# Kernel tuning notes

Hardware: AMD Instinct MI355X
Metric: run time of the kernel (lower is better)

## Reference

```python
import jax, jax.numpy as jnp
import numpy as np

N, E, F, H, C, G, NC = 50000, 800000, 128, 3, 64, 16, 10
NEG_SLOPE = 0.2


def gatv2_layer(x, src, dst, Wl, Wr, att, b, concat):
    # PyG GATv2Conv (share_weights=False, add_self_loops already in src/dst)
    n = x.shape[0]
    h, c = att.shape
    xl = (x @ Wl).reshape(n, h, c)   # source-side transform
    xr = (x @ Wr).reshape(n, h, c)   # target-side transform
    # per-edge attention logits: a^T LeakyReLU(xl_j + xr_i)
    e = jax.nn.leaky_relu(xl[src] + xr[dst], NEG_SLOPE)          # [E,h,c]
    logits = jnp.einsum('ehc,hc->eh', e, att)                    # [E,h]
    # segment softmax over incoming edges of each target node
    m = jax.ops.segment_max(logits, dst, num_segments=n)
    m = jnp.where(jnp.isfinite(m), m, jnp.zeros_like(m))
    p = jnp.exp(logits - m[dst])
    denom = jax.ops.segment_sum(p, dst, num_segments=n)
    alpha = p / jnp.maximum(denom[dst], 1e-16)                   # [E,h]
    out = jax.ops.segment_sum(alpha[:, :, None] * xl[src], dst, num_segments=n)
    out = out.reshape(n, h * c) if concat else out.mean(axis=1)
    return out + b


def setup_inputs() -> dict:
    key = jax.random.key(0)
    ks = jax.random.split(key, 16)
    glorot = lambda k, shp: jax.random.normal(k, shp, jnp.float32) * np.sqrt(2.0 / (shp[0] + shp[-1]))
    return {
        'x': jax.random.normal(ks[0], (N, F), jnp.float32),
        'edge_index': jax.random.randint(ks[1], (2, E), 0, N, jnp.int64),
        'batch': jnp.sort(jax.random.randint(ks[2], (N,), 0, G, jnp.int64)),
        'Wl1': glorot(ks[3], (F, H * C)),
        'Wr1': glorot(ks[4], (F, H * C)),
        'att1': glorot(ks[5], (H, C)),
        'b1': jnp.zeros((H * C,), jnp.float32),
        'Wl2': glorot(ks[6], (H * C, H * C)),
        'Wr2': glorot(ks[7], (H * C, H * C)),
        'att2': glorot(ks[8], (H, C)),
        'b2': jnp.zeros((C,), jnp.float32),
        'Wc': glorot(ks[9], (C, NC)),
        'bc': jnp.zeros((NC,), jnp.float32),
    }


def reference(x, edge_index, batch, Wl1, Wr1, att1, b1, Wl2, Wr2, att2, b2, Wc, bc):
    n = x.shape[0]
    loops = jnp.arange(n, dtype=edge_index.dtype)
    src = jnp.concatenate([edge_index[0], loops])  # add self loops (PyG default)
    dst = jnp.concatenate([edge_index[1], loops])
    h = jax.nn.relu(gatv2_layer(x, src, dst, Wl1, Wr1, att1, b1, True))
    # dropout is identity in eval mode
    h = jax.nn.relu(gatv2_layer(h, src, dst, Wl2, Wr2, att2, b2, False))
    # global mean pool over graph ids
    sums = jax.ops.segment_sum(h, batch, num_segments=G)
    counts = jax.ops.segment_sum(jnp.ones((n, 1), h.dtype), batch, num_segments=G)
    pooled = sums / jnp.maximum(counts, 1.0)
    logits = pooled @ Wc + bc
    return jax.nn.softmax(logits, axis=1)
```

## Files before the change

### kernel.cpp

```cpp
#include <hip/hip_runtime.h>
#include <hip/hip_bf16.h>
#include <stdint.h>

#define NN 50000
#define EE 800000
#define FF 128
#define HH 3
#define CC 64
#define GG 16
#define NCLS 10
#define HC (HH*CC)

#define LOG2E 1.4426950408889634f

typedef uint16_t u16;
typedef __attribute__((ext_vector_type(8))) short short8;
typedef __attribute__((ext_vector_type(4))) float f32x4;

__device__ __forceinline__ u16 bf16_rne(float x) {
    uint32_t u = __float_as_uint(x);
    u += 0x7fffu + ((u >> 16) & 1u);
    return (u16)(u >> 16);
}
__device__ __forceinline__ void split2(float x, u16& h, u16& l) {
    h = bf16_rne(x);
    float fh = __uint_as_float((uint32_t)h << 16);
    l = bf16_rne(x - fh);
}

__device__ __forceinline__ float qsum16(float x) {
    #define DPP_ADD(ctrl) \
        x += __int_as_float(__builtin_amdgcn_update_dpp(0, __float_as_int(x), ctrl, 0xf, 0xf, true))
    DPP_ADD(0x111);
    DPP_ADD(0x112);
    DPP_ADD(0x114);
    DPP_ADD(0x118);
    #undef DPP_ADD
    return __int_as_float(__builtin_amdgcn_ds_swizzle(__float_as_int(x), 0x1F0));
}

__device__ __forceinline__ void unpack12(uint4 q0, uint4 q1, float v[3][4]) {
    v[0][0] = __uint_as_float(q0.x << 16);
    v[1][0] = __uint_as_float(q0.x & 0xffff0000u);
    v[2][0] = __uint_as_float(q0.y << 16);
    v[0][1] = __uint_as_float(q0.z << 16);
    v[1][1] = __uint_as_float(q0.z & 0xffff0000u);
    v[2][1] = __uint_as_float(q0.w << 16);
    v[0][2] = __uint_as_float(q1.x << 16);
    v[1][2] = __uint_as_float(q1.x & 0xffff0000u);
    v[2][2] = __uint_as_float(q1.y << 16);
    v[0][3] = __uint_as_float(q1.z << 16);
    v[1][3] = __uint_as_float(q1.z & 0xffff0000u);
    v[2][3] = __uint_as_float(q1.w << 16);
}

__global__ void count_deg(const int* __restrict__ dst, int* __restrict__ deg, int E) {
    int i = blockIdx.x * blockDim.x + threadIdx.x;
    if (i < E) atomicAdd(&deg[dst[i]], 1);
}

__global__ __launch_bounds__(256) void scan_local(const int* __restrict__ deg,
                                                  int* __restrict__ rowp1,
                                                  int* __restrict__ partials, int n) {
    __shared__ int sums[256];
    int base = blockIdx.x * 2048 + threadIdx.x * 8;
    int v[8]; int run = 0;
    #pragma unroll
    for (int i = 0; i < 8; ++i) {
        int x = (base + i < n) ? deg[base + i] : 0;
        run += x; v[i] = run;
    }
    sums[threadIdx.x] = run;
    __syncthreads();
    for (int off = 1; off < 256; off <<= 1) {
        int t = (threadIdx.x >= off) ? sums[threadIdx.x - off] : 0;
        __syncthreads();
        sums[threadIdx.x] += t;
        __syncthreads();
    }
    int prefix = (threadIdx.x > 0) ? sums[threadIdx.x - 1] : 0;
    #pragma unroll
    for (int i = 0; i < 8; ++i)
        if (base + i < n) rowp1[base + i] = v[i] + prefix;
    if (threadIdx.x == 255) partials[blockIdx.x] = sums[255];
}

__global__ void scan_partials(int* partials, int nb) {
    if (threadIdx.x == 0 && blockIdx.x == 0) {
        int run = 0;
        for (int b = 0; b < nb; ++b) { int t = partials[b]; partials[b] = run; run += t; }
    }
}

__global__ void scan_finish(int* __restrict__ rowp, int* __restrict__ cursor,
                            const int* __restrict__ partials, int n) {
    int i = blockIdx.x * blockDim.x + threadIdx.x;
    if (i == 0) { rowp[0] = 0; cursor[0] = 0; }
    if (i < n) {
        int v = rowp[1 + i] + partials[i / 2048];
        rowp[1 + i] = v;
        if (i < n - 1) cursor[i + 1] = v;
    }
}

__global__ void fill_csr(const int* __restrict__ src, const int* __restrict__ dst,
                         int* __restrict__ cursor, int* __restrict__ colv, int E) {
    int i = blockIdx.x * blockDim.x + threadIdx.x;
    if (i < E) {
        int pos = atomicAdd(&cursor[dst[i]], 1);
        colv[pos] = src[i];
    }
}

__global__ void prep_all(const float* __restrict__ Wl1, const float* __restrict__ Wr1,
                         const float* __restrict__ Wl2, const float* __restrict__ Wr2,
                         u16* l1h, u16* l1l, u16* r1h, u16* r1l,
                         u16* l2h, u16* l2l, u16* r2h, u16* r2l) {
    int idx = blockIdx.x * blockDim.x + threadIdx.x;
    const int S1 = FF * HC, S2 = HC * HC;
    const float* B; u16 *H, *L; int K, f;
    if (idx < S1)                { B = Wl1; H = l1h; L = l1l; K = FF; f = idx; }
    else if (idx < 2*S1)         { B = Wr1; H = r1h; L = r1l; K = FF; f = idx - S1; }
    else if (idx < 2*S1 + S2)    { B = Wl2; H = l2h; L = l2l; K = HC; f = idx - 2*S1; }
    else if (idx < 2*S1 + 2*S2)  { B = Wr2; H = r2h; L = r2l; K = HC; f = idx - 2*S1 - S2; }
    else return;
    const int KB = K / 32;
    int j    = f & 7;
    int lane = (f >> 3) & 63;
    int rest = f >> 9;
    int kb    = rest % KB;
    int ntile = rest / KB;
    int n = ntile * 16 + (lane & 15);
    int k = kb * 32 + (lane >> 4) * 8 + j;
    u16 h, l; split2(B[k * HC + n], h, l);
    H[f] = h;
    L[f] = l;
}

template<int K, bool SPLITIN>
__global__ __launch_bounds__(256) void mfma_gemm(
    const float* __restrict__ Af,
    const u16* __restrict__ Ahi, const u16* __restrict__ Alo,
    const u16* __restrict__ B1h, const u16* __restrict__ B1l,
    const u16* __restrict__ B2h, const u16* __restrict__ B2l,
    u16* __restrict__ C1p, u16* __restrict__ C2p, int M)
{
    constexpr int KB  = K / 32;
    constexpr int NCH = K / 8;
    __shared__ __align__(16) u16 smem[64 * K * 2];
    u16* Ah = smem;
    u16* Al = smem + 64 * K;

    const int tid  = threadIdx.x;
    const int w    = tid >> 6;
    const int lane = tid & 63;
    const int m0   = blockIdx.x * 64;

    #pragma unroll
    for (int i = 0; i < (64 * NCH) / 256; ++i) {
        int id   = tid + 256 * i;
        int row  = id & 63;
        int c    = id >> 6;
        int rt   = row >> 4, frow = row & 15;
        int kb   = c >> 2,   fkc  = c & 3;
        int sw   = (rt ^ (rt << 1)) & 7;
        int slot = (fkc * 16 + frow) ^ sw;
        int laddr = ((rt * KB + kb) * 64 + slot) * 8;
        int grow = min(m0 + row, M - 1);
        if constexpr (SPLITIN) {
            float4 a0 = *(const float4*)(Af + (size_t)grow * K + c * 8);
            float4 a1 = *(const float4*)(Af + (size_t)grow * K + c * 8 + 4);
            ushort4 h0, l0, h1, l1;
            split2(a0.x, h0.x, l0.x); split2(a0.y, h0.y, l0.y);
            split2(a0.z, h0.z, l0.z); split2(a0.w, h0.w, l0.w);
            split2(a1.x, h1.x, l1.x); split2(a1.y, h1.y, l1.y);
            split2(a1.z, h1.z, l1.z); split2(a1.w, h1.w, l1.w);
            *(ushort4*)&Ah[laddr]     = h0;
            *(ushort4*)&Ah[laddr + 4] = h1;
            *(ushort4*)&Al[laddr]     = l0;
            *(ushort4*)&Al[laddr + 4] = l1;
        } else {
            *(uint4*)&Ah[laddr] = *(const uint4*)(Ahi + (size_t)grow * K + c * 8);
            *(uint4*)&Al[laddr] = *(const uint4*)(Alo + (size_t)grow * K + c * 8);
        }
    }
    __syncthreads();

    f32x4 acc[2][3][4];
    #pragma unroll
    for (int mt = 0; mt < 2; ++mt)
        #pragma unroll
        for (int nt = 0; nt < 3; ++nt)
            #pragma unroll
            for (int rt = 0; rt < 4; ++rt)
                acc[mt][nt][rt] = (f32x4){0.f, 0.f, 0.f, 0.f};

    const u16* bbase[2][3][2];
    #pragma unroll
    for (int mt = 0; mt < 2; ++mt) {
        const u16* Bh = mt ? B2h : B1h;
        const u16* Bl = mt ? B2l : B1l;
        #pragma unroll
        for (int nt = 0; nt < 3; ++nt) {
            size_t o = ((size_t)(w * 3 + nt) * KB * 64 + lane) * 8;
            bbase[mt][nt][0] = Bh + o;
            bbase[mt][nt][1] = Bl + o;
        }
    }

    #pragma unroll 2
    for (int kb = 0; kb < KB; ++kb) {
        short8 afh[4], afl[4];
        #pragma unroll
        for (int rt = 0; rt < 4; ++rt) {
            int sw = (rt ^ (rt << 1)) & 7;
            int laddr = ((rt * KB + kb) * 64 + (lane ^ sw)) * 8;
            afh[rt] = *(const short8*)&Ah[laddr];
            afl[rt] = *(const short8*)&Al[laddr];
        }
        #pragma unroll
        for (int mt = 0; mt < 2; ++mt) {
            #pragma unroll
            for (int nt = 0; nt < 3; ++nt) {
                short8 bh = *(const short8*)(bbase[mt][nt][0] + kb * 512);
                short8 bl = *(const short8*)(bbase[mt][nt][1] + kb * 512);
                #pragma unroll
                for (int rt = 0; rt < 4; ++rt)
                    acc[mt][nt][rt] = __builtin_amdgcn_mfma_f32_16x16x32_bf16(afh[rt], bh, acc[mt][nt][rt], 0, 0, 0);
                #pragma unroll
                for (int rt = 0; rt < 4; ++rt)
                    acc[mt][nt][rt] = __builtin_amdgcn_mfma_f32_16x16x32_bf16(afh[rt], bl, acc[mt][nt][rt], 0, 0, 0);
                #pragma unroll
                for (int rt = 0; rt < 4; ++rt)
                    acc[mt][nt][rt] = __builtin_amdgcn_mfma_f32_16x16x32_bf16(afl[rt], bh, acc[mt][nt][rt], 0, 0, 0);
            }
        }
    }

    const int frow = lane & 15;
    const int q4   = (lane >> 4) * 4;
    #pragma unroll
    for (int mt = 0; mt < 2; ++mt) {
        __syncthreads();
        #pragma unroll
        for (int nt = 0; nt < 3; ++nt) {
            int col = w * 48 + nt * 16 + frow;
            int c = col & 63, h = col >> 6;
            int u = c * 4 + h;
            int chunk = u >> 3, within = u & 7;
            #pragma unroll
            for (int rt = 0; rt < 4; ++rt)
                #pragma unroll
                for (int r = 0; r < 4; ++r) {
                    int lrow = rt * 16 + q4 + r;
                    smem[lrow * 256 + ((chunk ^ (lrow & 7)) << 3) + within] =
                        bf16_rne(acc[mt][nt][rt][r]);
                }
        }
        __syncthreads();
        u16* C = mt ? C2p : C1p;
        #pragma unroll
        for (int i = 0; i < 8; ++i) {
            int idx  = tid + 256 * i;
            int lrow = idx >> 5;
            int coff = idx & 31;
            if (m0 + lrow < M)
                *(uint4*)(C + (size_t)(m0 + lrow) * 256 + coff * 8) =
                    *(const uint4*)&smem[lrow * 256 + ((coff ^ (lrow & 7)) << 3)];
        }
    }
}

template<bool MASK>
__device__ __forceinline__ void gat_quad(
    int i0, int q, int l, int beg, int cnt, int cm1, int cmax, int node,
    const int* __restrict__ colv, const u16* __restrict__ xlp,
    const float attv[3][4], const float xrv[3][4],
    float s[3], float acc[3][4])
{
    int idx = i0 + q;
    int iq  = min(idx, cmax);
    int cs  = colv[beg + iq];
    int src = (idx < cm1) ? cs : node;
    const u16* p = xlp + ((size_t)src << 8) + (l << 4);
    uint4 q0 = *(const uint4*)p;
    uint4 q1 = *(const uint4*)(p + 8);
    float v[3][4];
    unpack12(q0, q1, v);
    #pragma unroll
    for (int r = 0; r < 3; ++r) {
        float t0 = v[r][0] + xrv[r][0]; t0 = fmaxf(t0, 0.2f * t0);
        float t1 = v[r][1] + xrv[r][1]; t1 = fmaxf(t1, 0.2f * t1);
        float t2 = v[r][2] + xrv[r][2]; t2 = fmaxf(t2, 0.2f * t2);
        float t3 = v[r][3] + xrv[r][3]; t3 = fmaxf(t3, 0.2f * t3);
        float d = t0 * attv[r][0];
        d = fmaf(t1, attv[r][1], d);
        d = fmaf(t2, attv[r][2], d);
        d = fmaf(t3, attv[r][3], d);
        d = qsum16(d);
        float pe = __builtin_amdgcn_exp2f(d);
        if (MASK) pe = (idx < cnt) ? pe : 0.f;
        s[r] += pe;
        acc[r][0] = fmaf(pe, v[r][0], acc[r][0]);
        acc[r][1] = fmaf(pe, v[r][1], acc[r][1]);
        acc[r][2] = fmaf(pe, v[r][2], acc[r][2]);
        acc[r][3] = fmaf(pe, v[r][3], acc[r][3]);
    }
}

template<int CONCAT>
__global__ __launch_bounds__(256) void gat_agg(
    const u16* __restrict__ xlp, const u16* __restrict__ xrp,
    const int* __restrict__ rowp, const int* __restrict__ colv,
    const float* __restrict__ att, const float* __restrict__ bias,
    float* __restrict__ out, u16* __restrict__ ohi, u16* __restrict__ olo, int n)
{
    const int wave = threadIdx.x >> 6;
    const int lane = threadIdx.x & 63;
    const int node = __builtin_amdgcn_readfirstlane(blockIdx.x * 4 + wave);
    if (node >= n) return;
    const int q = lane >> 4;
    const int l = lane & 15;

    float attv[3][4], xrv[3][4];
    #pragma unroll
    for (int r = 0; r < 3; ++r) {
        float4 a4 = *(const float4*)(att + r * 64 + 4 * l);
        attv[r][0] = a4.x * LOG2E; attv[r][1] = a4.y * LOG2E;
        attv[r][2] = a4.z * LOG2E; attv[r][3] = a4.w * LOG2E;
    }
    {
        uint4 x0 = *(const uint4*)(xrp + ((size_t)node << 8) + (l << 4));
        uint4 x1 = *(const uint4*)(xrp + ((size_t)node << 8) + (l << 4) + 8);
        unpack12(x0, x1, xrv);
    }

    float s[3] = {0.f, 0.f, 0.f};
    float acc[3][4] = {{0.f}};

    const int beg  = rowp[node];
    const int cnt  = rowp[node + 1] - beg + 1;
    const int cm1  = cnt - 1;
    const int cmax = max(cnt - 2, 0);

    int i0 = 0;
    const int nfull = cnt & ~3;
    for (; i0 < nfull; i0 += 4)
        gat_quad<false>(i0, q, l, beg, cnt, cm1, cmax, node, colv, xlp, attv, xrv, s, acc);
    if (i0 < cnt)
        gat_quad<true>(i0, q, l, beg, cnt, cm1, cmax, node, colv, xlp, attv, xrv, s, acc);

    #pragma unroll
    for (int r = 0; r < 3; ++r) {
        s[r] += __shfl_xor(s[r], 16, 64);
        s[r] += __shfl_xor(s[r], 32, 64);
        #pragma unroll
        for (int j = 0; j < 4; ++j) {
            acc[r][j] += __shfl_xor(acc[r][j], 16, 64);
            acc[r][j] += __shfl_xor(acc[r][j], 32, 64);
        }
    }

    if (CONCAT) {
        if (lane < 48) {
            int r = lane >> 4, ll = lane & 15;
            float inv = 1.f / s[r];
            float4 bv = *(const float4*)(bias + r * 64 + 4 * ll);
            ushort4 hv, lv;
            float o0 = fmaxf(fmaf(acc[r][0], inv, bv.x), 0.f); split2(o0, hv.x, lv.x);
            float o1 = fmaxf(fmaf(acc[r][1], inv, bv.y), 0.f); split2(o1, hv.y, lv.y);
            float o2 = fmaxf(fmaf(acc[r][2], inv, bv.z), 0.f); split2(o2, hv.z, lv.z);
            float o3 = fmaxf(fmaf(acc[r][3], inv, bv.w), 0.f); split2(o3, hv.w, lv.w);
            size_t ob = (size_t)node * HC + r * 64 + 4 * ll;
            *(ushort4*)&ohi[ob] = hv;
            *(ushort4*)&olo[ob] = lv;
        }
    } else {
        if (lane < 16) {
            float i0v = 1.f / s[0], i1v = 1.f / s[1], i2v = 1.f / s[2];
            float4 bv = *(const float4*)(bias + 4 * l);
            float4 o;
            o.x = fmaxf((acc[0][0]*i0v + acc[1][0]*i1v + acc[2][0]*i2v) * (1.f/3.f) + bv.x, 0.f);
            o.y = fmaxf((acc[0][1]*i0v + acc[1][1]*i1v + acc[2][1]*i2v) * (1.f/3.f) + bv.y, 0.f);
            o.z = fmaxf((acc[0][2]*i0v + acc[1][2]*i1v + acc[2][2]*i2v) * (1.f/3.f) + bv.z, 0.f);
            o.w = fmaxf((acc[0][3]*i0v + acc[1][3]*i1v + acc[2][3]*i2v) * (1.f/3.f) + bv.w, 0.f);
            *(float4*)&out[(size_t)node * CC + 4 * l] = o;
        }
    }
}

#define POOL_BLOCKS 384
__global__ __launch_bounds__(256) void pool_kernel(
    const float* __restrict__ h2, const int* __restrict__ batch,
    float* __restrict__ pool, float* __restrict__ cnt, int n)
{
    const int c   = threadIdx.x & 63;
    const int sub = threadIdx.x >> 6;
    const int per = (n + gridDim.x - 1) / gridDim.x;
    const int n0  = blockIdx.x * per;
    const int n1  = min(n0 + per, n);

    float run = 0.f;
    float crun = 0.f;
    int curg = -1;
    for (int node = n0 + sub; node < n1; node += 4) {
        int g = batch[node];
        if (g != curg) {
            if (curg >= 0) {
                atomicAdd(&pool[curg * CC + c], run);
                if (c == 0) atomicAdd(&cnt[curg], crun);
            }
            run = 0.f; crun = 0.f; curg = g;
        }
        run += h2[(size_t)node * CC + c];
        crun += 1.f;
    }
    if (curg >= 0) {
        atomicAdd(&pool[curg * CC + c], run);
        if (c == 0) atomicAdd(&cnt[curg], crun);
    }
}

__global__ void head_kernel(const float* __restrict__ pool, const float* __restrict__ cnt,
                            const float* __restrict__ Wc, const float* __restrict__ bc,
                            float* __restrict__ outp) {
    __shared__ float lg[GG][NCLS];
    int t = threadIdx.x;
    if (t < GG * NCLS) {
        int g = t / NCLS, k = t % NCLS;
        float invc = 1.f / fmaxf(cnt[g], 1.f);
        float a = 0.f;
        for (int c = 0; c < CC; ++c) a += pool[g * CC + c] * Wc[c * NCLS + k];
        lg[g][k] = a * invc + bc[k];
    }
    __syncthreads();
    if (t < GG) {
        float mx = -1e30f;
        for (int k = 0; k < NCLS; ++k) mx = fmaxf(mx, lg[t][k]);
        float ssum = 0.f; float e[NCLS];
        for (int k = 0; k < NCLS; ++k) { e[k] = __expf(lg[t][k] - mx); ssum += e[k]; }
        for (int k = 0; k < NCLS; ++k) outp[t * NCLS + k] = e[k] / ssum;
    }
}

extern "C" void kernel_launch(void* const* d_in, const int* in_sizes, int n_in,
                              void* d_out, int out_size, void* d_ws, size_t ws_size,
                              hipStream_t stream) {
    const float* x     = (const float*)d_in[0];
    const int*   ei    = (const int*)d_in[1];
    const int*   batch = (const int*)d_in[2];
    const float* Wl1   = (const float*)d_in[3];
    const float* Wr1   = (const float*)d_in[4];
    const float* att1  = (const float*)d_in[5];
    const float* b1    = (const float*)d_in[6];
    const float* Wl2   = (const float*)d_in[7];
    const float* Wr2   = (const float*)d_in[8];
    const float* att2  = (const float*)d_in[9];
    const float* b2    = (const float*)d_in[10];
    const float* Wc    = (const float*)d_in[11];
    const float* bc    = (const float*)d_in[12];

    const int n = in_sizes[2];
    const int E = in_sizes[1] / 2;
    const int* srcv = ei;
    const int* dstv = ei + E;

    char* base = (char*)d_ws;
    size_t off = 0;
    auto alloc = [&](size_t bytes) -> char* {
        char* p = base + off;
        off = (off + bytes + 255) & ~(size_t)255;
        return p;
    };
    int*   deg      = (int*)  alloc((size_t)n * 4);
    int*   cursor   = (int*)  alloc((size_t)n * 4);
    int*   rowp     = (int*)  alloc((size_t)(n + 1) * 4);
    int*   partials = (int*)  alloc(256 * 4);
    int*   colv     = (int*)  alloc((size_t)E * 4);
    u16*   xlp      = (u16*)  alloc((size_t)n * 256 * 2);
    u16*   xrp      = (u16*)  alloc((size_t)n * 256 * 2);
    u16*   bufHi    = (u16*)  alloc((size_t)n * HC * 2);
    u16*   bufLo    = (u16*)  alloc((size_t)n * HC * 2);
    float* h2       = (float*)alloc((size_t)n * CC * 4);
    float* pool     = (float*)alloc((size_t)GG * (CC + 1) * 4);
    float* cnt      = pool + GG * CC;
    u16*   Bl1hi    = (u16*)  alloc((size_t)FF * HC * 2);
    u16*   Bl1lo    = (u16*)  alloc((size_t)FF * HC * 2);
    u16*   Br1hi    = (u16*)  alloc((size_t)FF * HC * 2);
    u16*   Br1lo    = (u16*)  alloc((size_t)FF * HC * 2);
    u16*   Bl2hi    = (u16*)  alloc((size_t)HC * HC * 2);
    u16*   Bl2lo    = (u16*)  alloc((size_t)HC * HC * 2);
    u16*   Br2hi    = (u16*)  alloc((size_t)HC * HC * 2);
    u16*   Br2lo    = (u16*)  alloc((size_t)HC * HC * 2);

    hipMemsetAsync(deg, 0, (size_t)n * 4, stream);
    count_deg<<<(E + 255) / 256, 256, 0, stream>>>(dstv, deg, E);
    int nchunks = (n + 2047) / 2048;
    scan_local<<<nchunks, 256, 0, stream>>>(deg, rowp + 1, partials, n);
    scan_partials<<<1, 64, 0, stream>>>(partials, nchunks);
    scan_finish<<<(n + 255) / 256, 256, 0, stream>>>(rowp, cursor, partials, n);
    fill_csr<<<(E + 255) / 256, 256, 0, stream>>>(srcv, dstv, cursor, colv, E);

    const int prep_total = 2 * FF * HC + 2 * HC * HC;
    prep_all<<<(prep_total + 255) / 256, 256, 0, stream>>>(
        Wl1, Wr1, Wl2, Wr2, Bl1hi, Bl1lo, Br1hi, Br1lo, Bl2hi, Bl2lo, Br2hi, Br2lo);

    const int gblocks = (n + 63) / 64;

    mfma_gemm<FF, true><<<gblocks, 256, 0, stream>>>(
        x, nullptr, nullptr, Bl1hi, Bl1lo, Br1hi, Br1lo, xlp, xrp, n);
    gat_agg<1><<<(n + 3) / 4, 256, 0, stream>>>(xlp, xrp, rowp, colv, att1, b1,
                                                nullptr, bufHi, bufLo, n);

    mfma_gemm<HC, false><<<gblocks, 256, 0, stream>>>(
        nullptr, bufHi, bufLo, Bl2hi, Bl2lo, Br2hi, Br2lo, xlp, xrp, n);
    gat_agg<0><<<(n + 3) / 4, 256, 0, stream>>>(xlp, xrp, rowp, colv, att2, b2,
                                                h2, nullptr, nullptr, n);

    hipMemsetAsync(pool, 0, (size_t)GG * (CC + 1) * 4, stream);
    pool_kernel<<<POOL_BLOCKS, 256, 0, stream>>>(h2, batch, pool, cnt, n);
    head_kernel<<<1, 256, 0, stream>>>(pool, cnt, Wc, bc, (float*)d_out);
}
```

Measured before the change: 376.5 us.

## Pack xl/xr rows densely to 192 bf16 and store self loops in CSR

Drops the padded 256-element row layout for the transformed features and stores each node's 192 bf16 values contiguously, so the gather in aggregation reads 24 bytes per lane instead of 32. The GEMM epilogue writes 24 chunks per row instead of 32. Self loops become an explicit CSR entry (degree+1 in the scan plus an add_self kernel), which removes the per-edge select against the node index. The aggregation loop is also unrolled by 2. The cost is one extra small kernel launch, and the row loads are no longer aligned to power-of-two boundaries.

```diff
diff --git a/kernel.cpp b/kernel.cpp
--- a/kernel.cpp
+++ b/kernel.cpp
@@ -39,19 +39,19 @@
     return __int_as_float(__builtin_amdgcn_ds_swizzle(__float_as_int(x), 0x1F0));
 }
 
-__device__ __forceinline__ void unpack12(uint4 q0, uint4 q1, float v[3][4]) {
+__device__ __forceinline__ void unpack12(uint4 q0, uint2 q1, float v[3][4]) {
     v[0][0] = __uint_as_float(q0.x << 16);
     v[1][0] = __uint_as_float(q0.x & 0xffff0000u);
     v[2][0] = __uint_as_float(q0.y << 16);
-    v[0][1] = __uint_as_float(q0.z << 16);
-    v[1][1] = __uint_as_float(q0.z & 0xffff0000u);
-    v[2][1] = __uint_as_float(q0.w << 16);
-    v[0][2] = __uint_as_float(q1.x << 16);
-    v[1][2] = __uint_as_float(q1.x & 0xffff0000u);
-    v[2][2] = __uint_as_float(q1.y << 16);
-    v[0][3] = __uint_as_float(q1.z << 16);
-    v[1][3] = __uint_as_float(q1.z & 0xffff0000u);
-    v[2][3] = __uint_as_float(q1.w << 16);
+    v[0][1] = __uint_as_float(q0.y & 0xffff0000u);
+    v[1][1] = __uint_as_float(q0.z << 16);
+    v[2][1] = __uint_as_float(q0.z & 0xffff0000u);
+    v[0][2] = __uint_as_float(q0.w << 16);
+    v[1][2] = __uint_as_float(q0.w & 0xffff0000u);
+    v[2][2] = __uint_as_float(q1.x << 16);
+    v[0][3] = __uint_as_float(q1.x & 0xffff0000u);
+    v[1][3] = __uint_as_float(q1.y << 16);
+    v[2][3] = __uint_as_float(q1.y & 0xffff0000u);
 }
 
 __global__ void count_deg(const int* __restrict__ dst, int* __restrict__ deg, int E) {
@@ -67,7 +67,7 @@
     int v[8]; int run = 0;
     #pragma unroll
     for (int i = 0; i < 8; ++i) {
-        int x = (base + i < n) ? deg[base + i] : 0;
+        int x = (base + i < n) ? deg[base + i] + 1 : 0;
         run += x; v[i] = run;
     }
     sums[threadIdx.x] = run;
@@ -110,6 +110,11 @@
         int pos = atomicAdd(&cursor[dst[i]], 1);
         colv[pos] = src[i];
     }
+}
+
+__global__ void add_self(const int* __restrict__ rowp, int* __restrict__ colv, int n) {
+    int i = blockIdx.x * blockDim.x + threadIdx.x;
+    if (i < n) colv[rowp[i + 1] - 1] = i;
 }
 
 __global__ void prep_all(const float* __restrict__ Wl1, const float* __restrict__ Wr1,
@@ -246,7 +251,7 @@
         for (int nt = 0; nt < 3; ++nt) {
             int col = w * 48 + nt * 16 + frow;
             int c = col & 63, h = col >> 6;
-            int u = c * 4 + h;
+            int u = c * 3 + h;
             int chunk = u >> 3, within = u & 7;
             #pragma unroll
             for (int rt = 0; rt < 4; ++rt)
@@ -260,12 +265,12 @@
         __syncthreads();
         u16* C = mt ? C2p : C1p;
         #pragma unroll
-        for (int i = 0; i < 8; ++i) {
+        for (int i = 0; i < 6; ++i) {
             int idx  = tid + 256 * i;
-            int lrow = idx >> 5;
-            int coff = idx & 31;
+            int lrow = idx / 24;
+            int coff = idx % 24;
             if (m0 + lrow < M)
-                *(uint4*)(C + (size_t)(m0 + lrow) * 256 + coff * 8) =
+                *(uint4*)(C + (size_t)(m0 + lrow) * HC + coff * 8) =
                     *(const uint4*)&smem[lrow * 256 + ((coff ^ (lrow & 7)) << 3)];
         }
     }
@@ -273,18 +278,17 @@
 
 template<bool MASK>
 __device__ __forceinline__ void gat_quad(
-    int i0, int q, int l, int beg, int cnt, int cm1, int cmax, int node,
+    int i0, int q, int l, int beg, int cnt, int cm1,
     const int* __restrict__ colv, const u16* __restrict__ xlp,
     const float attv[3][4], const float xrv[3][4],
     float s[3], float acc[3][4])
 {
     int idx = i0 + q;
-    int iq  = min(idx, cmax);
-    int cs  = colv[beg + iq];
-    int src = (idx < cm1) ? cs : node;
-    const u16* p = xlp + ((size_t)src << 8) + (l << 4);
+    int iq  = MASK ? min(idx, cm1) : idx;
+    int src = colv[beg + iq];
+    const u16* p = xlp + (size_t)src * HC + l * 12;
     uint4 q0 = *(const uint4*)p;
-    uint4 q1 = *(const uint4*)(p + 8);
+    uint2 q1 = *(const uint2*)(p + 8);
     float v[3][4];
     unpack12(q0, q1, v);
     #pragma unroll
@@ -330,25 +334,26 @@
         attv[r][2] = a4.z * LOG2E; attv[r][3] = a4.w * LOG2E;
     }
     {
-        uint4 x0 = *(const uint4*)(xrp + ((size_t)node << 8) + (l << 4));
-        uint4 x1 = *(const uint4*)(xrp + ((size_t)node << 8) + (l << 4) + 8);
+        const u16* p = xrp + (size_t)node * HC + l * 12;
+        uint4 x0 = *(const uint4*)p;
+        uint2 x1 = *(const uint2*)(p + 8);
         unpack12(x0, x1, xrv);
     }
 
     float s[3] = {0.f, 0.f, 0.f};
     float acc[3][4] = {{0.f}};
 
-    const int beg  = rowp[node];
-    const int cnt  = rowp[node + 1] - beg + 1;
-    const int cm1  = cnt - 1;
-    const int cmax = max(cnt - 2, 0);
+    const int beg = rowp[node];
+    const int cnt = rowp[node + 1] - beg;
+    const int cm1 = cnt - 1;
 
     int i0 = 0;
     const int nfull = cnt & ~3;
+    #pragma unroll 2
     for (; i0 < nfull; i0 += 4)
-        gat_quad<false>(i0, q, l, beg, cnt, cm1, cmax, node, colv, xlp, attv, xrv, s, acc);
+        gat_quad<false>(i0, q, l, beg, cnt, cm1, colv, xlp, attv, xrv, s, acc);
     if (i0 < cnt)
-        gat_quad<true>(i0, q, l, beg, cnt, cm1, cmax, node, colv, xlp, attv, xrv, s, acc);
+        gat_quad<true>(i0, q, l, beg, cnt, cm1, colv, xlp, attv, xrv, s, acc);
 
     #pragma unroll
     for (int r = 0; r < 3; ++r) {
@@ -476,9 +481,9 @@
     int*   cursor   = (int*)  alloc((size_t)n * 4);
     int*   rowp     = (int*)  alloc((size_t)(n + 1) * 4);
     int*   partials = (int*)  alloc(256 * 4);
-    int*   colv     = (int*)  alloc((size_t)E * 4);
-    u16*   xlp      = (u16*)  alloc((size_t)n * 256 * 2);
-    u16*   xrp      = (u16*)  alloc((size_t)n * 256 * 2);
+    int*   colv     = (int*)  alloc((size_t)(E + n) * 4);
+    u16*   xlp      = (u16*)  alloc((size_t)n * HC * 2);
+    u16*   xrp      = (u16*)  alloc((size_t)n * HC * 2);
     u16*   bufHi    = (u16*)  alloc((size_t)n * HC * 2);
     u16*   bufLo    = (u16*)  alloc((size_t)n * HC * 2);
     float* h2       = (float*)alloc((size_t)n * CC * 4);
@@ -500,6 +505,7 @@
     scan_partials<<<1, 64, 0, stream>>>(partials, nchunks);
     scan_finish<<<(n + 255) / 256, 256, 0, stream>>>(rowp, cursor, partials, n);
     fill_csr<<<(E + 255) / 256, 256, 0, stream>>>(srcv, dstv, cursor, colv, E);
+    add_self<<<(n + 255) / 256, 256, 0, stream>>>(rowp, colv, n);
 
     const int prep_total = 2 * FF * HC + 2 * HC * HC;
     prep_all<<<(prep_total + 255) / 256, 256, 0, stream>>>(
```

Result: faster. 357.1 us (-5.1%).
